# Kernel optimization log

Measured on AMD Instinct MI355X. Metric: run time of the kernel, lower is better.

The kernel has to match this reference:

```python
import jax, jax.numpy as jnp
import numpy as np

N = 50000          # nodes
E = 3_200_000      # edges (radius-graph topology, avg degree ~64)
C = 10             # node channels
ED = 4             # edge_dim: [dist, dx, dy, food_flag]
H = 16             # message hidden dim
RADIUS = 0.05
ACC_SCALE = 0.005
MAX_VEL = 0.02
EDGES_TO_STAY_ALIVE = 3
CONSUMPTION_EDGES_REQUIRED = 3
NOISE_SCALE = 0.004


def setup_inputs() -> dict:
    key = jax.random.key(0)
    ks = jax.random.split(key, 10)
    pos = jax.random.uniform(ks[0], (N, 2), minval=-1.0, maxval=1.0)
    vel = jax.random.uniform(ks[1], (N, 2), minval=-MAX_VEL, maxval=MAX_VEL)
    # column 4: 1.0 = living cell, 0.0 = food node
    is_cell = (jax.random.uniform(ks[2], (N,)) > 0.2).astype(jnp.float32)
    hidden = jax.random.normal(ks[3], (N, C - 5)) * 0.1
    x = jnp.concatenate([pos, vel, is_cell[:, None], hidden], axis=1)  # [N,10]
    src = jax.random.randint(ks[4], (E,), 0, N)
    dst = jax.random.randint(ks[5], (E,), 0, N)
    noise = jax.random.uniform(ks[6], (N, 2))  # uniform [0,1), mapped to [-1,1) inside
    W_edge = jax.random.normal(ks[7], (ED, H)) * 0.3
    W_src = jax.random.normal(ks[8], (C, H)) * 0.3
    b1 = jnp.zeros((H,), jnp.float32)
    W_out = jax.random.normal(ks[9], (H, 4)) * 0.3
    b2 = jnp.zeros((4,), jnp.float32)
    return dict(x=x, src=src, dst=dst, noise=noise, W_edge=W_edge,
                W_src=W_src, b1=b1, W_out=W_out, b2=b2)


def reference(x, src, dst, noise, W_edge, W_src, b1, W_out, b2):
    pos = x[:, :2]
    vel = x[:, 2:4]
    cell = x[:, 4]
    c_mask = (cell == 1.0).astype(x.dtype)          # [N]

    # ---- edge attributes of the (dynamic) radius graph ----
    d = pos[src] - pos[dst]                          # [E,2] gather
    dist = jnp.sqrt(jnp.sum(d * d, axis=1) + 1e-12)  # [E]
    food_flag = cell[src]                            # 0 for food-source edges
    edge_attr = jnp.concatenate([dist[:, None], d, food_flag[:, None]], axis=1)  # [E,4]

    # ---- message passing: per-edge MLP + scatter-sum + node readout ----
    m = jax.nn.relu(edge_attr @ W_edge + x[src] @ W_src + b1)     # [E,H]
    agg = jax.ops.segment_sum(m, dst, num_segments=N)             # [N,H]
    h = jnp.tanh(agg @ W_out + b2) * c_mask[:, None]              # [N,4], masked as in update_graph

    # ---- velocity / position update ----
    acc = h[:, :2] * ACC_SCALE
    new_vel = jnp.clip(vel + acc, -MAX_VEL, MAX_VEL)
    new_pos = pos + new_vel                                       # wrap_around = False
    vel_noisy = new_vel + (noise * 2.0 - 1.0) * NOISE_SCALE * c_mask[:, None]
    new_x = jnp.concatenate(
        [new_pos, vel_noisy, cell[:, None], h[:, 2:], x[:, 7:]], axis=1)  # [N,10]

    # ---- costs / stats ----
    eps = 1e-6
    border_mask = (jnp.abs(new_pos) > 1.0).astype(x.dtype)        # [N,2]
    border_cost = jnp.sum(jnp.log(jnp.abs(new_pos) + eps) * border_mask)
    food_edge = (food_flag == 0.0)
    visible_food = food_edge.sum()
    mean_food_dist = jnp.sum(dist * food_edge.astype(x.dtype))

    # ---- node removal masks (jit-safe: return keep mask instead of slicing) ----
    deg = jax.ops.segment_sum(jnp.ones_like(dist), dst, num_segments=N)
    dead = (cell == 1.0) & (deg < EDGES_TO_STAY_ALIVE)
    consume_e = (dist < RADIUS) & (cell[src] == 1.0) & (cell[dst] == 0.0)
    cdeg = jax.ops.segment_sum(consume_e.astype(x.dtype), dst, num_segments=N)
    consumed = (cell == 0.0) & (cdeg >= CONSUMPTION_EDGES_REQUIRED)
    keep_mask = ~(dead | consumed)

    velocity_bonus = jnp.mean(jnp.abs(new_vel), axis=0)           # [2]
    dead_cost = dead.sum()
    food_reward = consumed.sum()
    return (new_x, keep_mask, velocity_bonus, border_cost, food_reward,
            dead_cost, visible_food, mean_food_dist)
```

## Files before the change

### kernel.cpp

```cpp
#include <hip/hip_runtime.h>
#include <hip/hip_fp16.h>
#include <math.h>

#define NN 50000
#define NE 3200000

#define NT    98
#define TSZ   512
#define CAP   34816
#define SCB   625
#define EPB   5120
#define EPT   20
#define NSL   8

static constexpr float ACC_SCALE   = 0.005f;
static constexpr float MAX_VEL     = 0.02f;
static constexpr float NOISE_SCALE = 0.004f;
static constexpr float RADIUS      = 0.05f;

#define OUT_KEEP   500000
#define OUT_SCAL   550000

#define WS_NI    0
#define WS_SREC  200704
#define WS_GCUR  802816
#define WS_BK    804416
#define WS_PACC  4216384
#define WS_PDEG  5822016

__global__ __launch_bounds__(256) void k1_prep(
    const float* __restrict__ x,
    const float* __restrict__ W_edge,
    const float* __restrict__ W_src,
    const float* __restrict__ b1,
    float4* __restrict__ nodeinfo,
    float4* __restrict__ srec,
    int* __restrict__ gcur,
    float* __restrict__ out_scalars)
{
    int n = blockIdx.x * 256 + threadIdx.x;
    if (blockIdx.x == 0) {
        if (threadIdx.x < 7) out_scalars[threadIdx.x] = 0.0f;
        for (int i = threadIdx.x; i < NT * 16; i += 256)
            gcur[i] = (i & 15) ? 0 : (i >> 4) * CAP;
    }
    if (n >= NN) return;

    float xr[10];
#pragma unroll
    for (int c = 0; c < 10; ++c) xr[c] = x[n * 10 + c];
    float cell = xr[4];

    nodeinfo[n] = make_float4(xr[0], xr[1], cell, 0.0f);

    float v[16];
#pragma unroll
    for (int j = 0; j < 16; ++j) {
        float a = fmaf(cell, W_edge[48 + j], b1[j]);
#pragma unroll
        for (int c = 0; c < 10; ++c) a = fmaf(xr[c], W_src[c * 16 + j], a);
        v[j] = a;
    }

    float4 r1, r2;
    r1.x = __builtin_bit_cast(float, __floats2half2_rn(v[0],  v[1]));
    r1.y = __builtin_bit_cast(float, __floats2half2_rn(v[2],  v[3]));
    r1.z = __builtin_bit_cast(float, __floats2half2_rn(v[4],  v[5]));
    r1.w = __builtin_bit_cast(float, __floats2half2_rn(v[6],  v[7]));
    r2.x = __builtin_bit_cast(float, __floats2half2_rn(v[8],  v[9]));
    r2.y = __builtin_bit_cast(float, __floats2half2_rn(v[10], v[11]));
    r2.z = __builtin_bit_cast(float, __floats2half2_rn(v[12], v[13]));
    r2.w = __builtin_bit_cast(float, __floats2half2_rn(v[14], v[15]));

    srec[(size_t)n * 3 + 0] = make_float4(xr[0], xr[1], cell, 0.0f);
    srec[(size_t)n * 3 + 1] = r1;
    srec[(size_t)n * 3 + 2] = r2;
}

__global__ __launch_bounds__(256) void k_scatter(
    const int* __restrict__ src,
    const int* __restrict__ dst,
    int* __restrict__ gcur,
    unsigned* __restrict__ bucket)
{
    __shared__ unsigned stage[EPB];
    __shared__ int hist[NT], binstart[NT], lcur[NT], gbase[NT];
    __shared__ int scanbuf[128];

    int tid = threadIdx.x;
    for (int i = tid; i < NT; i += 256) { hist[i] = 0; lcur[i] = 0; }
    __syncthreads();

    int e0 = blockIdx.x * EPB;

    int d[EPT];
#pragma unroll
    for (int j = 0; j < EPT; ++j) d[j] = dst[e0 + j * 256 + tid];
#pragma unroll
    for (int j = 0; j < EPT; ++j) atomicAdd(&hist[d[j] >> 9], 1);
    __syncthreads();

    if (tid < 128) scanbuf[tid] = (tid < NT) ? hist[tid] : 0;
    __syncthreads();
    for (int off = 1; off < 128; off <<= 1) {
        int v = 0;
        if (tid < 128 && tid >= off) v = scanbuf[tid - off];
        __syncthreads();
        if (tid < 128) scanbuf[tid] += v;
        __syncthreads();
    }
    if (tid < NT) {
        int tt = (tid + blockIdx.x) % NT;
        int bs = scanbuf[tt] - hist[tt];
        binstart[tt] = bs;
        gbase[tt] = atomicAdd(&gcur[tt * 16], hist[tt]) - bs;
    }
    __syncthreads();

    int sreg[EPT];
#pragma unroll
    for (int j = 0; j < EPT; ++j) sreg[j] = src[e0 + j * 256 + tid];
#pragma unroll
    for (int j = 0; j < EPT; ++j) {
        int t = d[j] >> 9;
        int pos = binstart[t] + atomicAdd(&lcur[t], 1);
        stage[pos] = (unsigned)sreg[j] | ((unsigned)(d[j] & 511) << 16)
                   | ((unsigned)t << 25);
    }
    __syncthreads();

#pragma unroll
    for (int j = 0; j < EPT; ++j) {
        int i = j * 256 + tid;
        unsigned e = stage[i];
        int b = e >> 25;
        int g = gbase[b] + i;
        if (g < (b + 1) * CAP) __builtin_nontemporal_store(e, &bucket[g]);
    }
}

__global__ __launch_bounds__(256) void k_agg(
    const float* __restrict__ W_edge,
    const float* __restrict__ W_out,
    const float4* __restrict__ nodeinfo,
    const float4* __restrict__ srec,
    const int* __restrict__ gcur,
    const unsigned* __restrict__ bucket,
    float4* __restrict__ pacc,
    int* __restrict__ pdeg,
    float* __restrict__ out_scalars)
{
    __shared__ float sAcc[TSZ][5];
    __shared__ int   sDeg[TSZ];
    __shared__ float sPX[TSZ], sPY[TSZ], sCL[TSZ];
    __shared__ float sRed[4][2];

    int t   = blockIdx.x >> 3;
    int sl  = blockIdx.x & 7;
    int tid = threadIdx.x;

    for (int j = tid; j < TSZ; j += 256) {
        int g = t * TSZ + j;
        float4 ni = (g < NN) ? nodeinfo[g] : make_float4(9e9f, 9e9f, -1.f, 0.f);
        sPX[j] = ni.x; sPY[j] = ni.y; sCL[j] = ni.z;
        sAcc[j][0] = 0.f; sAcc[j][1] = 0.f; sAcc[j][2] = 0.f; sAcc[j][3] = 0.f;
        sDeg[j] = 0;
    }

    float w0[16], w1[16], w2[16], woa[16], wob[16], woc[16], wod[16];
#pragma unroll
    for (int k = 0; k < 16; ++k) {
        w0[k] = W_edge[k];
        w1[k] = W_edge[16 + k];
        w2[k] = W_edge[32 + k];
        woa[k] = W_out[k * 4 + 0];
        wob[k] = W_out[k * 4 + 1];
        woc[k] = W_out[k * 4 + 2];
        wod[k] = W_out[k * 4 + 3];
    }
    __syncthreads();

    int cnt = gcur[t * 16] - t * CAP;
    if (cnt > CAP) cnt = CAP;
    int cs = (cnt + NSL - 1) / NSL;
    int i0 = sl * cs;
    int i1 = min(i0 + cs, cnt);

    const unsigned* bk = bucket + (size_t)t * CAP;
    float vis = 0.f, fd = 0.f;

#pragma unroll 4
    for (int i = i0 + tid; i < i1; i += 256) {
        unsigned e = __builtin_nontemporal_load(&bk[i]);
        int s  = e & 0xFFFF;
        int dl = (e >> 16) & 0x1FF;

        const float4* r = srec + (size_t)s * 3;
        float4 r0 = r[0];
        float4 r1 = r[1];
        float4 r2 = r[2];

        float dx = r0.x - sPX[dl];
        float dy = r0.y - sPY[dl];
        float dist = sqrtf(fmaf(dx, dx, fmaf(dy, dy, 1e-12f)));

        bool food0 = (r0.z == 0.0f);
        vis += food0 ? 1.f : 0.f;
        fd  += food0 ? dist : 0.f;

        bool consume = (dist < RADIUS) && (r0.z == 1.0f) && (sCL[dl] == 0.0f);
        atomicAdd(&sDeg[dl], consume ? 65537 : 1);

        float sv[16];
        {
            float2 f;
            f = __half22float2(__builtin_bit_cast(__half2, r1.x)); sv[0]=f.x;  sv[1]=f.y;
            f = __half22float2(__builtin_bit_cast(__half2, r1.y)); sv[2]=f.x;  sv[3]=f.y;
            f = __half22float2(__builtin_bit_cast(__half2, r1.z)); sv[4]=f.x;  sv[5]=f.y;
            f = __half22float2(__builtin_bit_cast(__half2, r1.w)); sv[6]=f.x;  sv[7]=f.y;
            f = __half22float2(__builtin_bit_cast(__half2, r2.x)); sv[8]=f.x;  sv[9]=f.y;
            f = __half22float2(__builtin_bit_cast(__half2, r2.y)); sv[10]=f.x; sv[11]=f.y;
            f = __half22float2(__builtin_bit_cast(__half2, r2.z)); sv[12]=f.x; sv[13]=f.y;
            f = __half22float2(__builtin_bit_cast(__half2, r2.w)); sv[14]=f.x; sv[15]=f.y;
        }

        float v0 = 0.f, v1 = 0.f, v2 = 0.f, v3 = 0.f;
#pragma unroll
        for (int k = 0; k < 16; ++k) {
            float m = fmaf(dist, w0[k], fmaf(dx, w1[k], fmaf(dy, w2[k], sv[k])));
            m = fmaxf(m, 0.0f);
            v0 = fmaf(m, woa[k], v0);
            v1 = fmaf(m, wob[k], v1);
            v2 = fmaf(m, woc[k], v2);
            v3 = fmaf(m, wod[k], v3);
        }
        atomicAdd(&sAcc[dl][0], v0);
        atomicAdd(&sAcc[dl][1], v1);
        atomicAdd(&sAcc[dl][2], v2);
        atomicAdd(&sAcc[dl][3], v3);
    }
    __syncthreads();

    for (int j = tid; j < TSZ; j += 256) {
        int o = sl * (NT * TSZ) + t * TSZ + j;
        pacc[o] = make_float4(sAcc[j][0], sAcc[j][1], sAcc[j][2], sAcc[j][3]);
        pdeg[o] = sDeg[j];
    }

#pragma unroll
    for (int off = 32; off > 0; off >>= 1) {
        vis += __shfl_down(vis, off);
        fd  += __shfl_down(fd,  off);
    }
    int lane = tid & 63, wv = tid >> 6;
    if (lane == 0) { sRed[wv][0] = vis; sRed[wv][1] = fd; }
    __syncthreads();
    if (tid == 0) {
        float a = 0.f, b = 0.f;
#pragma unroll
        for (int wq = 0; wq < 4; ++wq) { a += sRed[wq][0]; b += sRed[wq][1]; }
        atomicAdd(&out_scalars[5], a);
        atomicAdd(&out_scalars[6], b);
    }
}

__global__ __launch_bounds__(256) void k_final(
    const float* __restrict__ x,
    const float* __restrict__ noise,
    const float* __restrict__ b2,
    const float4* __restrict__ pacc,
    const int* __restrict__ pdeg,
    float* __restrict__ out,
    float* __restrict__ out_scalars)
{
    __shared__ float sRed[4][5];
    int tid  = threadIdx.x;
    int n    = blockIdx.x * 128 + (tid >> 1);
    int half = tid & 1;

    float a0 = 0.f, a1 = 0.f, a2 = 0.f, a3 = 0.f;
    int dp = 0;
    if (n < NN) {
#pragma unroll
        for (int sl = 0; sl < NSL / 2; ++sl) {
            int o = (2 * sl + half) * (NT * TSZ) + n;
            float4 q = pacc[o];
            a0 += q.x; a1 += q.y; a2 += q.z; a3 += q.w;
            dp += pdeg[o];
        }
    }
    a0 += __shfl_xor(a0, 1);
    a1 += __shfl_xor(a1, 1);
    a2 += __shfl_xor(a2, 1);
    a3 += __shfl_xor(a3, 1);
    dp += __shfl_xor(dp, 1);

    float avx = 0.f, avy = 0.f, bc = 0.f, deadf = 0.f, consf = 0.f;
    if (n < NN && half == 0) {
        float cell = x[n * 10 + 4];
        float cm = (cell == 1.0f) ? 1.0f : 0.0f;
        float h0 = tanhf(a0 + b2[0]) * cm;
        float h1 = tanhf(a1 + b2[1]) * cm;
        float h2 = tanhf(a2 + b2[2]) * cm;
        float h3 = tanhf(a3 + b2[3]) * cm;

        float px = x[n * 10 + 0], py = x[n * 10 + 1];
        float vx = x[n * 10 + 2], vy = x[n * 10 + 3];

        float nvx = fminf(fmaxf(fmaf(h0, ACC_SCALE, vx), -MAX_VEL), MAX_VEL);
        float nvy = fminf(fmaxf(fmaf(h1, ACC_SCALE, vy), -MAX_VEL), MAX_VEL);
        float npx = px + nvx;
        float npy = py + nvy;

        float vnx = nvx + (noise[n * 2 + 0] * 2.0f - 1.0f) * NOISE_SCALE * cm;
        float vny = nvy + (noise[n * 2 + 1] * 2.0f - 1.0f) * NOISE_SCALE * cm;

        float* row = out + (size_t)n * 10;
        row[0] = npx;  row[1] = npy;
        row[2] = vnx;  row[3] = vny;
        row[4] = cell; row[5] = h2;  row[6] = h3;
        row[7] = x[n * 10 + 7];
        row[8] = x[n * 10 + 8];
        row[9] = x[n * 10 + 9];

        float apx = fabsf(npx), apy = fabsf(npy);
        if (apx > 1.0f) bc += logf(apx + 1e-6f);
        if (apy > 1.0f) bc += logf(apy + 1e-6f);

        int deg  = dp & 0xFFFF;
        int cdeg = dp >> 16;
        bool dead = (cell == 1.0f) && (deg < 3);
        bool cons = (cell == 0.0f) && (cdeg >= 3);
        out[OUT_KEEP + n] = (dead || cons) ? 0.0f : 1.0f;
        deadf = dead ? 1.0f : 0.0f;
        consf = cons ? 1.0f : 0.0f;
        avx = fabsf(nvx) * (1.0f / NN);
        avy = fabsf(nvy) * (1.0f / NN);
    }

    float r[5] = { avx, avy, bc, consf, deadf };
#pragma unroll
    for (int q = 0; q < 5; ++q) {
#pragma unroll
        for (int off = 32; off > 0; off >>= 1)
            r[q] += __shfl_down(r[q], off);
    }
    int lane = tid & 63, wv = tid >> 6;
    if (lane == 0) {
#pragma unroll
        for (int q = 0; q < 5; ++q) sRed[wv][q] = r[q];
    }
    __syncthreads();
    if (tid == 0) {
#pragma unroll
        for (int q = 0; q < 5; ++q) {
            float acc = sRed[0][q] + sRed[1][q] + sRed[2][q] + sRed[3][q];
            atomicAdd(&out_scalars[q], acc);
        }
    }
}

extern "C" void kernel_launch(void* const* d_in, const int* in_sizes, int n_in,
                              void* d_out, int out_size, void* d_ws, size_t ws_size,
                              hipStream_t stream) {
    const float* x      = (const float*)d_in[0];
    const int*   src    = (const int*)  d_in[1];
    const int*   dst    = (const int*)  d_in[2];
    const float* noise  = (const float*)d_in[3];
    const float* W_edge = (const float*)d_in[4];
    const float* W_src  = (const float*)d_in[5];
    const float* b1     = (const float*)d_in[6];
    const float* W_out  = (const float*)d_in[7];
    const float* b2     = (const float*)d_in[8];

    float* ws = (float*)d_ws;
    float4*   nodeinfo = (float4*)(ws + WS_NI);
    float4*   srec     = (float4*)(ws + WS_SREC);
    int*      gcur     = (int*)(ws + WS_GCUR);
    unsigned* bucket   = (unsigned*)(ws + WS_BK);
    float4*   pacc     = (float4*)(ws + WS_PACC);
    int*      pdeg     = (int*)(ws + WS_PDEG);

    float* out         = (float*)d_out;
    float* out_scalars = out + OUT_SCAL;

    k1_prep<<<196, 256, 0, stream>>>(
        x, W_edge, W_src, b1, nodeinfo, srec, gcur, out_scalars);

    k_scatter<<<SCB, 256, 0, stream>>>(src, dst, gcur, bucket);

    k_agg<<<NT * NSL, 256, 0, stream>>>(
        W_edge, W_out, nodeinfo, srec, gcur, bucket, pacc, pdeg, out_scalars);

    k_final<<<392, 256, 0, stream>>>(
        x, noise, b2, pacc, pdeg, out, out_scalars);
}
```

Measured before the change: 229.2 us.

## Retile destination bins, batch gathers four-deep, drop nodeinfo buffer

Changes the destination tiling from 98 bins of 512 nodes to 128 bins of 392 nodes, with 6 slices per bin and a smaller bucket capacity. The aggregation loop now issues four bucket loads and twelve source-record gathers before processing them, which raises memory-level parallelism. It also sets launch bounds for two blocks per CU and removes the separate nodeinfo array by reading positions from the first float4 of srec. Risks include more register pressure from the batched loads, integer division by a non-power-of-two tile size in the scatter kernel, and bucket overflow if a bin exceeds the reduced capacity.

New measurement: 218.3 us. 1.05x faster.

```diff
diff --git a/kernel.cpp b/kernel.cpp
--- a/kernel.cpp
+++ b/kernel.cpp
@@ -5,13 +5,13 @@
 #define NN 50000
 #define NE 3200000
 
-#define NT    98
-#define TSZ   512
-#define CAP   34816
+#define NT    128
+#define TSZ   392
+#define CAP   26624
 #define SCB   625
 #define EPB   5120
 #define EPT   20
-#define NSL   8
+#define NSL   6
 
 static constexpr float ACC_SCALE   = 0.005f;
 static constexpr float MAX_VEL     = 0.02f;
@@ -21,19 +21,17 @@
 #define OUT_KEEP   500000
 #define OUT_SCAL   550000
 
-#define WS_NI    0
-#define WS_SREC  200704
-#define WS_GCUR  802816
-#define WS_BK    804416
-#define WS_PACC  4216384
-#define WS_PDEG  5822016
+#define WS_SREC  0
+#define WS_GCUR  602112
+#define WS_BK    604160
+#define WS_PACC  4012032
+#define WS_PDEG  5216256
 
 __global__ __launch_bounds__(256) void k1_prep(
     const float* __restrict__ x,
     const float* __restrict__ W_edge,
     const float* __restrict__ W_src,
     const float* __restrict__ b1,
-    float4* __restrict__ nodeinfo,
     float4* __restrict__ srec,
     int* __restrict__ gcur,
     float* __restrict__ out_scalars)
@@ -51,8 +49,6 @@
     for (int c = 0; c < 10; ++c) xr[c] = x[n * 10 + c];
     float cell = xr[4];
 
-    nodeinfo[n] = make_float4(xr[0], xr[1], cell, 0.0f);
-
     float v[16];
 #pragma unroll
     for (int j = 0; j < 16; ++j) {
@@ -97,10 +93,10 @@
 #pragma unroll
     for (int j = 0; j < EPT; ++j) d[j] = dst[e0 + j * 256 + tid];
 #pragma unroll
-    for (int j = 0; j < EPT; ++j) atomicAdd(&hist[d[j] >> 9], 1);
-    __syncthreads();
-
-    if (tid < 128) scanbuf[tid] = (tid < NT) ? hist[tid] : 0;
+    for (int j = 0; j < EPT; ++j) atomicAdd(&hist[d[j] / TSZ], 1);
+    __syncthreads();
+
+    if (tid < 128) scanbuf[tid] = hist[tid];
     __syncthreads();
     for (int off = 1; off < 128; off <<= 1) {
         int v = 0;
@@ -109,8 +105,8 @@
         if (tid < 128) scanbuf[tid] += v;
         __syncthreads();
     }
-    if (tid < NT) {
-        int tt = (tid + blockIdx.x) % NT;
+    if (tid < 128) {
+        int tt = (tid + blockIdx.x) & 127;
         int bs = scanbuf[tt] - hist[tt];
         binstart[tt] = bs;
         gbase[tt] = atomicAdd(&gcur[tt * 16], hist[tt]) - bs;
@@ -122,9 +118,10 @@
     for (int j = 0; j < EPT; ++j) sreg[j] = src[e0 + j * 256 + tid];
 #pragma unroll
     for (int j = 0; j < EPT; ++j) {
-        int t = d[j] >> 9;
+        int t  = d[j] / TSZ;
+        int dl = d[j] - t * TSZ;
         int pos = binstart[t] + atomicAdd(&lcur[t], 1);
-        stage[pos] = (unsigned)sreg[j] | ((unsigned)(d[j] & 511) << 16)
+        stage[pos] = (unsigned)sreg[j] | ((unsigned)dl << 16)
                    | ((unsigned)t << 25);
     }
     __syncthreads();
@@ -139,10 +136,9 @@
     }
 }
 
-__global__ __launch_bounds__(256) void k_agg(
+__global__ __launch_bounds__(256, 2) void k_agg(
     const float* __restrict__ W_edge,
     const float* __restrict__ W_out,
-    const float4* __restrict__ nodeinfo,
     const float4* __restrict__ srec,
     const int* __restrict__ gcur,
     const unsigned* __restrict__ bucket,
@@ -155,13 +151,14 @@
     __shared__ float sPX[TSZ], sPY[TSZ], sCL[TSZ];
     __shared__ float sRed[4][2];
 
-    int t   = blockIdx.x >> 3;
-    int sl  = blockIdx.x & 7;
+    int t   = blockIdx.x / NSL;
+    int sl  = blockIdx.x - t * NSL;
     int tid = threadIdx.x;
 
     for (int j = tid; j < TSZ; j += 256) {
         int g = t * TSZ + j;
-        float4 ni = (g < NN) ? nodeinfo[g] : make_float4(9e9f, 9e9f, -1.f, 0.f);
+        float4 ni = (g < NN) ? srec[(size_t)g * 3]
+                             : make_float4(9e9f, 9e9f, -1.f, 0.f);
         sPX[j] = ni.x; sPY[j] = ni.y; sCL[j] = ni.z;
         sAcc[j][0] = 0.f; sAcc[j][1] = 0.f; sAcc[j][2] = 0.f; sAcc[j][3] = 0.f;
         sDeg[j] = 0;
@@ -182,47 +179,36 @@
 
     int cnt = gcur[t * 16] - t * CAP;
     if (cnt > CAP) cnt = CAP;
-    int cs = (cnt + NSL - 1) / NSL;
-    int i0 = sl * cs;
-    int i1 = min(i0 + cs, cnt);
+    int per = (cnt + NSL - 1) / NSL;
+    int i0 = sl * per;
+    int i1 = min(i0 + per, cnt);
 
     const unsigned* bk = bucket + (size_t)t * CAP;
     float vis = 0.f, fd = 0.f;
 
-#pragma unroll 4
-    for (int i = i0 + tid; i < i1; i += 256) {
-        unsigned e = __builtin_nontemporal_load(&bk[i]);
-        int s  = e & 0xFFFF;
+    auto PROC = [&](unsigned e, float4 A, float4 B, float4 C) {
         int dl = (e >> 16) & 0x1FF;
-
-        const float4* r = srec + (size_t)s * 3;
-        float4 r0 = r[0];
-        float4 r1 = r[1];
-        float4 r2 = r[2];
-
-        float dx = r0.x - sPX[dl];
-        float dy = r0.y - sPY[dl];
+        float dx = A.x - sPX[dl];
+        float dy = A.y - sPY[dl];
         float dist = sqrtf(fmaf(dx, dx, fmaf(dy, dy, 1e-12f)));
 
-        bool food0 = (r0.z == 0.0f);
+        bool food0 = (A.z == 0.0f);
         vis += food0 ? 1.f : 0.f;
         fd  += food0 ? dist : 0.f;
 
-        bool consume = (dist < RADIUS) && (r0.z == 1.0f) && (sCL[dl] == 0.0f);
+        bool consume = (dist < RADIUS) && (A.z == 1.0f) && (sCL[dl] == 0.0f);
         atomicAdd(&sDeg[dl], consume ? 65537 : 1);
 
         float sv[16];
-        {
-            float2 f;
-            f = __half22float2(__builtin_bit_cast(__half2, r1.x)); sv[0]=f.x;  sv[1]=f.y;
-            f = __half22float2(__builtin_bit_cast(__half2, r1.y)); sv[2]=f.x;  sv[3]=f.y;
-            f = __half22float2(__builtin_bit_cast(__half2, r1.z)); sv[4]=f.x;  sv[5]=f.y;
-            f = __half22float2(__builtin_bit_cast(__half2, r1.w)); sv[6]=f.x;  sv[7]=f.y;
-            f = __half22float2(__builtin_bit_cast(__half2, r2.x)); sv[8]=f.x;  sv[9]=f.y;
-            f = __half22float2(__builtin_bit_cast(__half2, r2.y)); sv[10]=f.x; sv[11]=f.y;
-            f = __half22float2(__builtin_bit_cast(__half2, r2.z)); sv[12]=f.x; sv[13]=f.y;
-            f = __half22float2(__builtin_bit_cast(__half2, r2.w)); sv[14]=f.x; sv[15]=f.y;
-        }
+        float2 f;
+        f = __half22float2(__builtin_bit_cast(__half2, B.x)); sv[0]=f.x;  sv[1]=f.y;
+        f = __half22float2(__builtin_bit_cast(__half2, B.y)); sv[2]=f.x;  sv[3]=f.y;
+        f = __half22float2(__builtin_bit_cast(__half2, B.z)); sv[4]=f.x;  sv[5]=f.y;
+        f = __half22float2(__builtin_bit_cast(__half2, B.w)); sv[6]=f.x;  sv[7]=f.y;
+        f = __half22float2(__builtin_bit_cast(__half2, C.x)); sv[8]=f.x;  sv[9]=f.y;
+        f = __half22float2(__builtin_bit_cast(__half2, C.y)); sv[10]=f.x; sv[11]=f.y;
+        f = __half22float2(__builtin_bit_cast(__half2, C.z)); sv[12]=f.x; sv[13]=f.y;
+        f = __half22float2(__builtin_bit_cast(__half2, C.w)); sv[14]=f.x; sv[15]=f.y;
 
         float v0 = 0.f, v1 = 0.f, v2 = 0.f, v3 = 0.f;
 #pragma unroll
@@ -238,6 +224,33 @@
         atomicAdd(&sAcc[dl][1], v1);
         atomicAdd(&sAcc[dl][2], v2);
         atomicAdd(&sAcc[dl][3], v3);
+    };
+
+#pragma unroll 1
+    for (int base = i0 + tid; base < i1; base += 1024) {
+        int iend = i1 - 1;
+        int j1 = min(base + 256, iend);
+        int j2 = min(base + 512, iend);
+        int j3 = min(base + 768, iend);
+
+        unsigned e0 = __builtin_nontemporal_load(&bk[base]);
+        unsigned e1 = __builtin_nontemporal_load(&bk[j1]);
+        unsigned e2 = __builtin_nontemporal_load(&bk[j2]);
+        unsigned e3 = __builtin_nontemporal_load(&bk[j3]);
+
+        const float4* p0 = srec + (size_t)(e0 & 0xFFFF) * 3;
+        const float4* p1 = srec + (size_t)(e1 & 0xFFFF) * 3;
+        const float4* p2 = srec + (size_t)(e2 & 0xFFFF) * 3;
+        const float4* p3 = srec + (size_t)(e3 & 0xFFFF) * 3;
+        float4 A0 = p0[0], B0 = p0[1], C0 = p0[2];
+        float4 A1 = p1[0], B1 = p1[1], C1 = p1[2];
+        float4 A2 = p2[0], B2 = p2[1], C2 = p2[2];
+        float4 A3 = p3[0], B3 = p3[1], C3 = p3[2];
+
+        PROC(e0, A0, B0, C0);
+        if (base + 256 < i1) PROC(e1, A1, B1, C1);
+        if (base + 512 < i1) PROC(e2, A2, B2, C2);
+        if (base + 768 < i1) PROC(e3, A3, B3, C3);
     }
     __syncthreads();
 
@@ -282,8 +295,8 @@
     int dp = 0;
     if (n < NN) {
 #pragma unroll
-        for (int sl = 0; sl < NSL / 2; ++sl) {
-            int o = (2 * sl + half) * (NT * TSZ) + n;
+        for (int k = 0; k < NSL / 2; ++k) {
+            int o = (2 * k + half) * (NT * TSZ) + n;
             float4 q = pacc[o];
             a0 += q.x; a1 += q.y; a2 += q.z; a3 += q.w;
             dp += pdeg[o];
@@ -374,23 +387,22 @@
     const float* b2     = (const float*)d_in[8];
 
     float* ws = (float*)d_ws;
-    float4*   nodeinfo = (float4*)(ws + WS_NI);
-    float4*   srec     = (float4*)(ws + WS_SREC);
-    int*      gcur     = (int*)(ws + WS_GCUR);
-    unsigned* bucket   = (unsigned*)(ws + WS_BK);
-    float4*   pacc     = (float4*)(ws + WS_PACC);
-    int*      pdeg     = (int*)(ws + WS_PDEG);
+    float4*   srec   = (float4*)(ws + WS_SREC);
+    int*      gcur   = (int*)(ws + WS_GCUR);
+    unsigned* bucket = (unsigned*)(ws + WS_BK);
+    float4*   pacc   = (float4*)(ws + WS_PACC);
+    int*      pdeg   = (int*)(ws + WS_PDEG);
 
     float* out         = (float*)d_out;
     float* out_scalars = out + OUT_SCAL;
 
     k1_prep<<<196, 256, 0, stream>>>(
-        x, W_edge, W_src, b1, nodeinfo, srec, gcur, out_scalars);
+        x, W_edge, W_src, b1, srec, gcur, out_scalars);
 
     k_scatter<<<SCB, 256, 0, stream>>>(src, dst, gcur, bucket);
 
     k_agg<<<NT * NSL, 256, 0, stream>>>(
-        W_edge, W_out, nodeinfo, srec, gcur, bucket, pacc, pdeg, out_scalars);
+        W_edge, W_out, srec, gcur, bucket, pacc, pdeg, out_scalars);
 
     k_final<<<392, 256, 0, stream>>>(
         x, noise, b2, pacc, pdeg, out, out_scalars);
```
